# Kernel optimization log

Hardware: AMD Instinct MI355X
Metric: run time of the kernel (lower is better)

The kernel has to match this reference:

```python
import jax, jax.numpy as jnp
import numpy as np

TEMPERATURE = 0.5
EPS = 1e-8  # torch F.cosine_similarity eps


def _neg_mask_indices(two_b):
    """Static row/col indices replicating sim[mask].view(2B, -1).
    Mask excludes the diagonal and the (i, B+i)/(B+i, i) positive pairs,
    leaving exactly 2B-2 entries per row, extracted in row-major order."""
    b = two_b // 2
    mask = np.ones((two_b, two_b), dtype=bool)
    np.fill_diagonal(mask, False)
    i = np.arange(b)
    mask[i, b + i] = False
    mask[b + i, i] = False
    rows, cols = np.nonzero(mask)
    return rows.reshape(two_b, two_b - 2), cols.reshape(two_b, two_b - 2)


def setup_inputs() -> dict:
    key = jax.random.key(0)
    k1, k2 = jax.random.split(key)
    two_b, d = 8192, 128
    embeddings = jax.random.normal(k1, (two_b, d), dtype=jnp.float32)
    labels = jax.random.randint(k2, (two_b,), 0, two_b - 2)
    return {"embeddings": embeddings, "labels": labels}


def reference(embeddings, labels):
    two_b = embeddings.shape[0]
    # cosine similarity via normalize + matmul (same math as the broadcast
    # F.cosine_similarity, without the O(N^2*D) intermediate)
    norms = jnp.linalg.norm(embeddings, axis=1)  # [2B]
    sim = (embeddings @ embeddings.T) / jnp.maximum(norms[:, None] * norms[None, :], EPS)
    sim = sim / TEMPERATURE  # [2B, 2B]
    rows, cols = _neg_mask_indices(two_b)
    logits = sim[rows, cols]  # [2B, 2B-2]
    # CrossEntropyLoss(reduction='sum') then / (2B)
    logz = jax.nn.logsumexp(logits, axis=1)  # [2B]
    picked = jnp.take_along_axis(logits, labels[:, None].astype(jnp.int32), axis=1)[:, 0]
    loss = jnp.sum(logz - picked) / two_b
    return loss
```

## Files before the change

kernel.cpp:

```cpp
#include <hip/hip_runtime.h>
#include <hip/hip_bf16.h>


typedef __bf16 bf16x8 __attribute__((ext_vector_type(8)));
typedef float floatx4 __attribute__((ext_vector_type(4)));

#define TWO_B 8192
#define B_HALF 4096
#define D 128
#define INV_T 2.0f
#define FIXED_MAX 2.0f
#define C_EXP 2.885390081777927f

#if defined(__has_builtin) && __has_builtin(__builtin_amdgcn_exp2f)
#define EXP2F(x) __builtin_amdgcn_exp2f(x)
#else
#define EXP2F(x) exp2f(x)
#endif
#if defined(__has_builtin) && __has_builtin(__builtin_amdgcn_logf)
#define LOG2F(x) __builtin_amdgcn_logf(x)
#else
#define LOG2F(x) log2f(x)
#endif

__device__ inline void load16_lds(const __bf16* g, __bf16* l) {
    __builtin_amdgcn_global_load_lds(
        (const __attribute__((address_space(1))) unsigned int*)g,
        (__attribute__((address_space(3))) unsigned int*)l, 16, 0, 0);
}

__global__ void k_prep(const float* __restrict__ emb,
                       const int* __restrict__ labels,
                       __bf16* __restrict__ nb,
                       float* __restrict__ picked,
                       float* __restrict__ l_arr) {
    int wv   = threadIdx.x >> 6;
    int lane = threadIdx.x & 63;
    int i = blockIdx.x * 4 + wv;
    const float2* e2 = reinterpret_cast<const float2*>(emb + (size_t)i * D);
    float2 v = e2[lane];
    float ssi = v.x * v.x + v.y * v.y;
    int p = i ^ B_HALF;
    int a = min(i, p), b = max(i, p);
    int l = labels[i];
    int c = l + (l >= a);
    c += (c >= b);
    const float2* ec2 = reinterpret_cast<const float2*>(emb + (size_t)c * D);
    float2 u = ec2[lane];
    float dot = v.x * u.x + v.y * u.y;
    float ssc = u.x * u.x + u.y * u.y;
#pragma unroll
    for (int off = 32; off >= 1; off >>= 1) {
        ssi += __shfl_xor(ssi, off, 64);
        dot += __shfl_xor(dot, off, 64);
        ssc += __shfl_xor(ssc, off, 64);
    }
    float rn = rsqrtf(fmaxf(ssi, 1e-16f));
    union { __bf16 h[2]; unsigned int uu; } pk;
    pk.h[0] = (__bf16)(v.x * rn);
    pk.h[1] = (__bf16)(v.y * rn);
    reinterpret_cast<unsigned int*>(nb)[i * 64 + lane] = pk.uu;
    if (lane == 0)
        picked[i] = dot / fmaxf(sqrtf(ssi * ssc), 1e-8f) * INV_T;
    if (blockIdx.x < TWO_B / 256) l_arr[blockIdx.x * 256 + threadIdx.x] = 0.f;
}

__global__ __launch_bounds__(256, 2) void k_gemm(const __bf16* __restrict__ nb,
                                                 float* __restrict__ l_arr) {
    __shared__ __bf16 lds[2][16384];

    const int bi = blockIdx.x;
    const int g  = blockIdx.y;

    const int lane = threadIdx.x & 63;
    const int w    = threadIdx.x >> 6;
    const int m    = lane & 15;
    const int quad = lane >> 4;
    const int row0 = bi * 128 + w * 32;

    bf16x8 a0[4], a1[4];
#pragma unroll
    for (int kc = 0; kc < 4; ++kc) {
        a0[kc] = *reinterpret_cast<const bf16x8*>(
            nb + (size_t)(row0 + m) * D + kc * 32 + quad * 8);
        a1[kc] = *reinterpret_cast<const bf16x8*>(
            nb + (size_t)(row0 + 16 + m) * D + kc * 32 + quad * 8);
    }
    asm volatile("" : "+v"(a0[0]), "+v"(a0[1]), "+v"(a0[2]), "+v"(a0[3]),
                      "+v"(a1[0]), "+v"(a1[1]), "+v"(a1[2]), "+v"(a1[3]));

    float l0[4] = {0.f, 0.f, 0.f, 0.f};
    float l1[4] = {0.f, 0.f, 0.f, 0.f};
    const int i0 = row0 + quad * 4;

    const int by0 = g;
    const int bj0 = (bi + by0) & 63;
    const bool has1 = (g + 17 <= 32) && !((g + 17 == 32) && (bi >= 32));
    const int by1 = g + 17;
    const int bj1 = (bi + by1) & 63;

    {
        const __bf16* gp0 = nb + (size_t)(bj0 * 128 + m) * D + w * 32 + quad * 8;
#pragma unroll
        for (int j = 0; j < 8; ++j)
            load16_lds(gp0 + (size_t)j * 16 * D, &lds[0][j * 2048 + w * 512]);
        if (has1) {
            const __bf16* gp1 = nb + (size_t)(bj1 * 128 + m) * D + w * 32 + quad * 8;
#pragma unroll
            for (int j = 0; j < 8; ++j)
                load16_lds(gp1 + (size_t)j * 16 * D, &lds[1][j * 2048 + w * 512]);
        }
    }
    __builtin_amdgcn_sched_barrier(0);

    auto compute_strip = [&](int C0, bool isdiag, bool bmask, const __bf16* buf) {
#pragma unroll
        for (int grp = 0; grp < 2; ++grp) {
            floatx4 acc0[4] = {{0.f,0.f,0.f,0.f},{0.f,0.f,0.f,0.f},
                               {0.f,0.f,0.f,0.f},{0.f,0.f,0.f,0.f}};
            floatx4 acc1[4] = {{0.f,0.f,0.f,0.f},{0.f,0.f,0.f,0.f},
                               {0.f,0.f,0.f,0.f},{0.f,0.f,0.f,0.f}};
#pragma unroll
            for (int kc = 0; kc < 4; ++kc) {
                const bf16x8 a0k = a0[kc], a1k = a1[kc];
#pragma unroll
                for (int s = 0; s < 4; ++s) {
                    bf16x8 b = *reinterpret_cast<const bf16x8*>(
                        &buf[((grp * 4 + s) * 4 + kc) * 512 + lane * 8]);
                    acc0[s] = __builtin_amdgcn_mfma_f32_16x16x32_bf16(a0k, b, acc0[s], 0, 0, 0);
                    acc1[s] = __builtin_amdgcn_mfma_f32_16x16x32_bf16(a1k, b, acc1[s], 0, 0, 0);
                }
            }
#pragma unroll
            for (int s = 0; s < 4; ++s) {
                const int jj = C0 + (grp * 4 + s) * 16 + m;
                float cs = 0.f;
                if (bmask) {
#pragma unroll
                    for (int r = 0; r < 4; ++r) {
                        float e0 = EXP2F(fmaf(acc0[s][r], C_EXP, -C_EXP));
                        float e1 = EXP2F(fmaf(acc1[s][r], C_EXP, -C_EXP));
                        if (((jj ^ (i0 + r)) & ~B_HALF) == 0) e0 = 0.f;
                        if (((jj ^ (i0 + 16 + r)) & ~B_HALF) == 0) e1 = 0.f;
                        l0[r] += e0;
                        l1[r] += e1;
                        cs += e0 + e1;
                    }
                } else {
#pragma unroll
                    for (int r = 0; r < 4; ++r) {
                        float e0 = EXP2F(fmaf(acc0[s][r], C_EXP, -C_EXP));
                        float e1 = EXP2F(fmaf(acc1[s][r], C_EXP, -C_EXP));
                        l0[r] += e0;
                        l1[r] += e1;
                        cs += e0 + e1;
                    }
                }
                if (!isdiag) {
                    cs += __shfl_xor(cs, 16, 64);
                    cs += __shfl_xor(cs, 32, 64);
                    if (quad == 0) atomicAdd(&l_arr[jj], cs);
                }
            }
        }
    };

    if (has1) { asm volatile("s_waitcnt vmcnt(8)" ::: "memory"); }
    else      { asm volatile("s_waitcnt vmcnt(0)" ::: "memory"); }
    __builtin_amdgcn_s_barrier();
    __builtin_amdgcn_sched_barrier(0);
    compute_strip(bj0 * 128, by0 == 0, (by0 == 0) || (by0 == 32), &lds[0][0]);

    if (has1) {
        asm volatile("s_waitcnt vmcnt(0)" ::: "memory");
        __builtin_amdgcn_s_barrier();
        __builtin_amdgcn_sched_barrier(0);
        compute_strip(bj1 * 128, false, (by1 == 32), &lds[1][0]);
    }

#pragma unroll
    for (int r = 0; r < 4; ++r) {
        float s = l0[r];
        s += __shfl_xor(s, 1, 64);
        s += __shfl_xor(s, 2, 64);
        s += __shfl_xor(s, 4, 64);
        s += __shfl_xor(s, 8, 64);
        if (m == 0) atomicAdd(&l_arr[i0 + r], s);
    }
#pragma unroll
    for (int r = 0; r < 4; ++r) {
        float s = l1[r];
        s += __shfl_xor(s, 1, 64);
        s += __shfl_xor(s, 2, 64);
        s += __shfl_xor(s, 4, 64);
        s += __shfl_xor(s, 8, 64);
        if (m == 0) atomicAdd(&l_arr[i0 + 16 + r], s);
    }
}

__global__ void k_final(const float* __restrict__ l_arr,
                        const float* __restrict__ picked,
                        float* __restrict__ out) {
    __shared__ float sred[16];
    float s = 0.f;
#pragma unroll
    for (int k = 0; k < TWO_B / 1024; ++k) {
        int i = threadIdx.x + k * 1024;
        s += FIXED_MAX + LOG2F(l_arr[i]) * 0.6931471805599453f - picked[i];
    }
#pragma unroll
    for (int off = 32; off >= 1; off >>= 1) s += __shfl_xor(s, off, 64);
    if ((threadIdx.x & 63) == 0) sred[threadIdx.x >> 6] = s;
    __syncthreads();
    if (threadIdx.x == 0) {
        float t = 0.f;
#pragma unroll
        for (int k = 0; k < 16; ++k) t += sred[k];
        out[0] = t * (1.0f / TWO_B);
    }
}

extern "C" void kernel_launch(void* const* d_in, const int* in_sizes, int n_in,
                              void* d_out, int out_size, void* d_ws, size_t ws_size,
                              hipStream_t stream) {
    const float* emb    = (const float*)d_in[0];
    const int*   labels = (const int*)d_in[1];
    char* ws = (char*)d_ws;
    float*  l_arr  = (float*)ws;
    float*  picked = (float*)(ws + 32768);
    __bf16* nb     = (__bf16*)(ws + 65536);
    float*  out    = (float*)d_out;

    k_prep<<<TWO_B / 4, 256, 0, stream>>>(emb, labels, nb, picked, l_arr);
    dim3 g2(64, 17);
    k_gemm<<<g2, 256, 0, stream>>>(nb, l_arr);
    k_final<<<1, 1024, 0, stream>>>(l_arr, picked, out);
}
```

Before: 88.53 us.

## Pipeline half-tile staging in GEMM and fuse final reduction via last-block counter

Splits each 128-column B strip into two 64-column halves held in a smaller LDS buffer pair. The next half is prefetched while the current half's MFMA epilogue runs, and the smaller LDS footprint allows launch bounds of 4 blocks per CU instead of 2. The separate k_final launch is removed. The last GEMM block, found through an atomic counter reset in k_prep, now does the log-sum and loss reduction. This removes one kernel launch and overlaps loads with exp work, at the cost of more barriers, manual vmcnt bookkeeping and a serialized tail in one block.

```diff
diff --git a/kernel.cpp b/kernel.cpp
--- a/kernel.cpp
+++ b/kernel.cpp
@@ -11,6 +11,7 @@
 #define INV_T 2.0f
 #define FIXED_MAX 2.0f
 #define C_EXP 2.885390081777927f
+#define NBLK (64 * 17)
 
 #if defined(__has_builtin) && __has_builtin(__builtin_amdgcn_exp2f)
 #define EXP2F(x) __builtin_amdgcn_exp2f(x)
@@ -33,7 +34,8 @@
                        const int* __restrict__ labels,
                        __bf16* __restrict__ nb,
                        float* __restrict__ picked,
-                       float* __restrict__ l_arr) {
+                       float* __restrict__ l_arr,
+                       unsigned int* __restrict__ cnt) {
     int wv   = threadIdx.x >> 6;
     int lane = threadIdx.x & 63;
     int i = blockIdx.x * 4 + wv;
@@ -63,11 +65,17 @@
     if (lane == 0)
         picked[i] = dot / fmaxf(sqrtf(ssi * ssc), 1e-8f) * INV_T;
     if (blockIdx.x < TWO_B / 256) l_arr[blockIdx.x * 256 + threadIdx.x] = 0.f;
-}
-
-__global__ __launch_bounds__(256, 2) void k_gemm(const __bf16* __restrict__ nb,
-                                                 float* __restrict__ l_arr) {
-    __shared__ __bf16 lds[2][16384];
+    if (blockIdx.x == 0 && threadIdx.x == 0) *cnt = 0u;
+}
+
+__global__ __launch_bounds__(256, 4) void k_gemm(const __bf16* __restrict__ nb,
+                                                 float* __restrict__ l_arr,
+                                                 const float* __restrict__ picked,
+                                                 float* __restrict__ out,
+                                                 unsigned int* __restrict__ cnt) {
+    __shared__ __bf16 lds[2][8192];
+    __shared__ unsigned int last_flag;
+    __shared__ float fred[4];
 
     const int bi = blockIdx.x;
     const int g  = blockIdx.y;
@@ -93,89 +101,122 @@
     float l1[4] = {0.f, 0.f, 0.f, 0.f};
     const int i0 = row0 + quad * 4;
 
-    const int by0 = g;
-    const int bj0 = (bi + by0) & 63;
-    const bool has1 = (g + 17 <= 32) && !((g + 17 == 32) && (bi >= 32));
-    const int by1 = g + 17;
-    const int bj1 = (bi + by1) & 63;
-
-    {
-        const __bf16* gp0 = nb + (size_t)(bj0 * 128 + m) * D + w * 32 + quad * 8;
-#pragma unroll
-        for (int j = 0; j < 8; ++j)
-            load16_lds(gp0 + (size_t)j * 16 * D, &lds[0][j * 2048 + w * 512]);
-        if (has1) {
-            const __bf16* gp1 = nb + (size_t)(bj1 * 128 + m) * D + w * 32 + quad * 8;
-#pragma unroll
-            for (int j = 0; j < 8; ++j)
-                load16_lds(gp1 + (size_t)j * 16 * D, &lds[1][j * 2048 + w * 512]);
-        }
-    }
-    __builtin_amdgcn_sched_barrier(0);
-
-    auto compute_strip = [&](int C0, bool isdiag, bool bmask, const __bf16* buf) {
-#pragma unroll
-        for (int grp = 0; grp < 2; ++grp) {
-            floatx4 acc0[4] = {{0.f,0.f,0.f,0.f},{0.f,0.f,0.f,0.f},
-                               {0.f,0.f,0.f,0.f},{0.f,0.f,0.f,0.f}};
-            floatx4 acc1[4] = {{0.f,0.f,0.f,0.f},{0.f,0.f,0.f,0.f},
-                               {0.f,0.f,0.f,0.f},{0.f,0.f,0.f,0.f}};
-#pragma unroll
-            for (int kc = 0; kc < 4; ++kc) {
-                const bf16x8 a0k = a0[kc], a1k = a1[kc];
-#pragma unroll
-                for (int s = 0; s < 4; ++s) {
-                    bf16x8 b = *reinterpret_cast<const bf16x8*>(
-                        &buf[((grp * 4 + s) * 4 + kc) * 512 + lane * 8]);
-                    acc0[s] = __builtin_amdgcn_mfma_f32_16x16x32_bf16(a0k, b, acc0[s], 0, 0, 0);
-                    acc1[s] = __builtin_amdgcn_mfma_f32_16x16x32_bf16(a1k, b, acc1[s], 0, 0, 0);
-                }
-            }
-#pragma unroll
-            for (int s = 0; s < 4; ++s) {
-                const int jj = C0 + (grp * 4 + s) * 16 + m;
-                float cs = 0.f;
-                if (bmask) {
-#pragma unroll
-                    for (int r = 0; r < 4; ++r) {
-                        float e0 = EXP2F(fmaf(acc0[s][r], C_EXP, -C_EXP));
-                        float e1 = EXP2F(fmaf(acc1[s][r], C_EXP, -C_EXP));
-                        if (((jj ^ (i0 + r)) & ~B_HALF) == 0) e0 = 0.f;
-                        if (((jj ^ (i0 + 16 + r)) & ~B_HALF) == 0) e1 = 0.f;
-                        l0[r] += e0;
-                        l1[r] += e1;
-                        cs += e0 + e1;
-                    }
-                } else {
-#pragma unroll
-                    for (int r = 0; r < 4; ++r) {
-                        float e0 = EXP2F(fmaf(acc0[s][r], C_EXP, -C_EXP));
-                        float e1 = EXP2F(fmaf(acc1[s][r], C_EXP, -C_EXP));
-                        l0[r] += e0;
-                        l1[r] += e1;
-                        cs += e0 + e1;
-                    }
-                }
-                if (!isdiag) {
-                    cs += __shfl_xor(cs, 16, 64);
-                    cs += __shfl_xor(cs, 32, 64);
-                    if (quad == 0) atomicAdd(&l_arr[jj], cs);
-                }
+    const int  bj0   = (bi + g) & 63;
+    const bool diag0 = (g == 0);
+    const bool has1  = (g < 15) || (g == 15 && bi < 32);
+    const int  bj1   = (bi + g + 17) & 63;
+    const bool bmask1 = (g == 15);
+
+    __bf16* buf0 = &lds[0][0];
+    __bf16* buf1 = &lds[1][0];
+
+    auto stage_half = [&](int bj, int h, __bf16* buf) {
+        const __bf16* gp = nb + (size_t)(bj * 128 + h * 64 + m) * D + w * 32 + quad * 8;
+#pragma unroll
+        for (int j = 0; j < 4; ++j)
+            load16_lds(gp + (size_t)j * 16 * D, &buf[j * 2048 + w * 512]);
+    };
+
+    auto mfma_half = [&](const __bf16* buf, floatx4 (&A0)[4], floatx4 (&A1)[4]) {
+#pragma unroll
+        for (int j = 0; j < 4; ++j) { A0[j] = {0.f,0.f,0.f,0.f}; A1[j] = {0.f,0.f,0.f,0.f}; }
+#pragma unroll
+        for (int kc = 0; kc < 4; ++kc) {
+            const bf16x8 a0k = a0[kc], a1k = a1[kc];
+#pragma unroll
+            for (int j = 0; j < 4; ++j) {
+                bf16x8 b = *reinterpret_cast<const bf16x8*>(
+                    &buf[(j * 4 + kc) * 512 + lane * 8]);
+                A0[j] = __builtin_amdgcn_mfma_f32_16x16x32_bf16(a0k, b, A0[j], 0, 0, 0);
+                A1[j] = __builtin_amdgcn_mfma_f32_16x16x32_bf16(a1k, b, A1[j], 0, 0, 0);
             }
         }
     };
 
-    if (has1) { asm volatile("s_waitcnt vmcnt(8)" ::: "memory"); }
-    else      { asm volatile("s_waitcnt vmcnt(0)" ::: "memory"); }
-    __builtin_amdgcn_s_barrier();
+    auto epi_half = [&](int c0h, bool bmask, bool isdiag,
+                        floatx4 (&A0)[4], floatx4 (&A1)[4]) {
+#pragma unroll
+        for (int j = 0; j < 4; ++j) {
+            const int jj = c0h + j * 16 + m;
+            float cs = 0.f;
+            if (bmask) {
+#pragma unroll
+                for (int r = 0; r < 4; ++r) {
+                    float e0 = EXP2F(fmaf(A0[j][r], C_EXP, -C_EXP));
+                    float e1 = EXP2F(fmaf(A1[j][r], C_EXP, -C_EXP));
+                    if (((jj ^ (i0 + r)) & ~B_HALF) == 0) e0 = 0.f;
+                    if (((jj ^ (i0 + 16 + r)) & ~B_HALF) == 0) e1 = 0.f;
+                    l0[r] += e0;
+                    l1[r] += e1;
+                    cs += e0 + e1;
+                }
+            } else {
+#pragma unroll
+                for (int r = 0; r < 4; ++r) {
+                    float e0 = EXP2F(fmaf(A0[j][r], C_EXP, -C_EXP));
+                    float e1 = EXP2F(fmaf(A1[j][r], C_EXP, -C_EXP));
+                    l0[r] += e0;
+                    l1[r] += e1;
+                    cs += e0 + e1;
+                }
+            }
+            cs += __shfl_xor(cs, 16, 64);
+            cs += __shfl_xor(cs, 32, 64);
+            if (isdiag) cs = 0.f;
+            if (quad == 0) atomicAdd(&l_arr[jj], cs);
+        }
+    };
+
+    floatx4 acc0[4], acc1[4];
+
+    stage_half(bj0, 0, buf0);
+    stage_half(bj0, 1, buf1);
     __builtin_amdgcn_sched_barrier(0);
-    compute_strip(bj0 * 128, by0 == 0, (by0 == 0) || (by0 == 32), &lds[0][0]);
 
     if (has1) {
-        asm volatile("s_waitcnt vmcnt(0)" ::: "memory");
-        __builtin_amdgcn_s_barrier();
-        __builtin_amdgcn_sched_barrier(0);
-        compute_strip(bj1 * 128, false, (by1 == 32), &lds[1][0]);
+        asm volatile("s_waitcnt vmcnt(4)" ::: "memory");
+        __builtin_amdgcn_s_barrier();
+        __builtin_amdgcn_sched_barrier(0);
+        mfma_half(buf0, acc0, acc1);
+        __builtin_amdgcn_sched_barrier(0);
+        __builtin_amdgcn_s_barrier();
+        stage_half(bj1, 0, buf0);
+        __builtin_amdgcn_sched_barrier(0);
+        epi_half(bj0 * 128, diag0, diag0, acc0, acc1);
+        asm volatile("s_waitcnt vmcnt(8)" ::: "memory");
+        __builtin_amdgcn_s_barrier();
+        __builtin_amdgcn_sched_barrier(0);
+        mfma_half(buf1, acc0, acc1);
+        __builtin_amdgcn_sched_barrier(0);
+        __builtin_amdgcn_s_barrier();
+        stage_half(bj1, 1, buf1);
+        __builtin_amdgcn_sched_barrier(0);
+        epi_half(bj0 * 128 + 64, diag0, diag0, acc0, acc1);
+        asm volatile("s_waitcnt vmcnt(12)" ::: "memory");
+        __builtin_amdgcn_s_barrier();
+        __builtin_amdgcn_sched_barrier(0);
+        mfma_half(buf0, acc0, acc1);
+        __builtin_amdgcn_sched_barrier(0);
+        epi_half(bj1 * 128, bmask1, false, acc0, acc1);
+        asm volatile("s_waitcnt vmcnt(8)" ::: "memory");
+        __builtin_amdgcn_s_barrier();
+        __builtin_amdgcn_sched_barrier(0);
+        mfma_half(buf1, acc0, acc1);
+        __builtin_amdgcn_sched_barrier(0);
+        epi_half(bj1 * 128 + 64, bmask1, false, acc0, acc1);
+    } else {
+        asm volatile("s_waitcnt vmcnt(4)" ::: "memory");
+        __builtin_amdgcn_s_barrier();
+        __builtin_amdgcn_sched_barrier(0);
+        mfma_half(buf0, acc0, acc1);
+        __builtin_amdgcn_sched_barrier(0);
+        epi_half(bj0 * 128, false, false, acc0, acc1);
+        asm volatile("s_waitcnt vmcnt(4)" ::: "memory");
+        __builtin_amdgcn_s_barrier();
+        __builtin_amdgcn_sched_barrier(0);
+        mfma_half(buf1, acc0, acc1);
+        __builtin_amdgcn_sched_barrier(0);
+        epi_half(bj0 * 128 + 64, false, false, acc0, acc1);
     }
 
 #pragma unroll
@@ -196,27 +237,27 @@
         s += __shfl_xor(s, 8, 64);
         if (m == 0) atomicAdd(&l_arr[i0 + 16 + r], s);
     }
-}
-
-__global__ void k_final(const float* __restrict__ l_arr,
-                        const float* __restrict__ picked,
-                        float* __restrict__ out) {
-    __shared__ float sred[16];
-    float s = 0.f;
-#pragma unroll
-    for (int k = 0; k < TWO_B / 1024; ++k) {
-        int i = threadIdx.x + k * 1024;
-        s += FIXED_MAX + LOG2F(l_arr[i]) * 0.6931471805599453f - picked[i];
-    }
-#pragma unroll
-    for (int off = 32; off >= 1; off >>= 1) s += __shfl_xor(s, off, 64);
-    if ((threadIdx.x & 63) == 0) sred[threadIdx.x >> 6] = s;
+
+    __threadfence();
+    if (threadIdx.x == 0)
+        last_flag = (atomicAdd(cnt, 1u) == (unsigned)NBLK - 1u) ? 1u : 0u;
     __syncthreads();
-    if (threadIdx.x == 0) {
-        float t = 0.f;
-#pragma unroll
-        for (int k = 0; k < 16; ++k) t += sred[k];
-        out[0] = t * (1.0f / TWO_B);
+    if (last_flag) {
+        __threadfence();
+        float s = 0.f;
+#pragma unroll
+        for (int k2 = 0; k2 < TWO_B / 256; ++k2) {
+            int i = threadIdx.x + k2 * 256;
+            float lv = __hip_atomic_load(&l_arr[i], __ATOMIC_RELAXED,
+                                         __HIP_MEMORY_SCOPE_AGENT);
+            s += FIXED_MAX + LOG2F(lv) * 0.6931471805599453f - picked[i];
+        }
+#pragma unroll
+        for (int off = 32; off >= 1; off >>= 1) s += __shfl_xor(s, off, 64);
+        if (lane == 0) fred[w] = s;
+        __syncthreads();
+        if (threadIdx.x == 0)
+            out[0] = (fred[0] + fred[1] + fred[2] + fred[3]) * (1.0f / TWO_B);
     }
 }
 
@@ -226,13 +267,13 @@
     const float* emb    = (const float*)d_in[0];
     const int*   labels = (const int*)d_in[1];
     char* ws = (char*)d_ws;
-    float*  l_arr  = (float*)ws;
-    float*  picked = (float*)(ws + 32768);
-    __bf16* nb     = (__bf16*)(ws + 65536);
-    float*  out    = (float*)d_out;
-
-    k_prep<<<TWO_B / 4, 256, 0, stream>>>(emb, labels, nb, picked, l_arr);
+    float*        l_arr  = (float*)ws;
+    float*        picked = (float*)(ws + 32768);
+    unsigned int* cnt    = (unsigned int*)(ws + 65536);
+    __bf16*       nb     = (__bf16*)(ws + 69632);
+    float*        out    = (float*)d_out;
+
+    k_prep<<<TWO_B / 4, 256, 0, stream>>>(emb, labels, nb, picked, l_arr, cnt);
     dim3 g2(64, 17);
-    k_gemm<<<g2, 256, 0, stream>>>(nb, l_arr);
-    k_final<<<1, 1024, 0, stream>>>(l_arr, picked, out);
-}
+    k_gemm<<<g2, 256, 0, stream>>>(nb, l_arr, picked, out, cnt);
+}
```

Result: slower. 189.8 us (+114.4%).
